# Kernel tuning notes

Measured on AMD Instinct MI355X. Metric: run time of the kernel, lower is better.

## Reference

```python
import jax, jax.numpy as jnp
import numpy as np

# ---- static config (mirrors HashEncoderHyFluid.__init__) ----
MIN_RES = np.array([16, 16, 16, 16], dtype=np.float64)
MAX_RES = np.array([256, 256, 256, 128], dtype=np.float64)
NUM_SCALES = 16
MAX_PARAMS = 2 ** 19
F = 2  # features_per_level
N_QUERIES = 1_000_000
PRIMES = np.array([1, 2654435761, 805459861, 3674653429], dtype=np.uint32)
# 16 corner offsets of the 4D hypercube, bit d of idx selects low/high along dim d
BITS = np.array([[(i >> d) & 1 for d in range(4)] for i in range(16)], dtype=np.int32)  # (16,4)


def build_config():
    b = np.exp((np.log(MAX_RES) - np.log(MIN_RES)) / (NUM_SCALES - 1))
    shapes, sizes, indicators, offsets = [], [], [], []
    total = 0
    for s in range(NUM_SCALES):
        res = np.ceil(MIN_RES * np.power(b, s)).astype(np.int64)
        raw = int(res[0] + 1) * int(res[1] + 1) * int(res[2] + 1) * int(res[3] + 1)
        p = raw if raw % 8 == 0 else ((raw + 7) // 8) * 8
        p = min(MAX_PARAMS, p)
        shapes.append(res)
        sizes.append(p)
        indicators.append(1 if raw <= p else 0)
        offsets.append(total)
        total += p * F
    return shapes, sizes, indicators, offsets, total


SHAPES, SIZES, INDICATORS, OFFSETS, TOTAL_HASH_SIZE = build_config()  # total = 15205344


def setup_inputs() -> dict:
    key = jax.random.key(0)
    k1, k2 = jax.random.split(key)
    xyzt = jax.random.uniform(k1, (N_QUERIES, 4), dtype=jnp.float32)  # coords in [0,1)
    hash_table = (jax.random.uniform(k2, (TOTAL_HASH_SIZE,), dtype=jnp.float32) * 2.0 - 1.0) * 0.001
    return {"xyzt": xyzt, "hash_table": hash_table}


def _encode_scale(xyzt, hash_table, res, size, indicator, offset):
    # xyzt: (N,4) in [0,1]; res: np int64 (4,)
    resf = jnp.asarray(res.astype(np.float32))
    pos = xyzt * resf                      # (N,4) grid-space position
    grid = jnp.floor(pos)
    frac = pos - grid                      # (N,4)
    grid = grid.astype(jnp.int32)
    corners = grid[:, None, :] + jnp.asarray(BITS)[None, :, :]          # (N,16,4)
    hi = jnp.asarray(BITS, jnp.float32)[None, :, :]                     # (1,16,4)
    w = jnp.prod(hi * frac[:, None, :] + (1.0 - hi) * (1.0 - frac[:, None, :]), axis=-1)  # (N,16)
    cu = corners.astype(jnp.uint32)
    if indicator == 1:
        # dense linear indexing: strides = cumprod(res+1), wrapping at uint32 like taichi
        strides = np.cumprod(np.concatenate([[1], (res + 1)[:3]])).astype(np.uint32)
        idx = jnp.sum(cu * jnp.asarray(strides), axis=-1)               # (N,16) uint32, wraps
    else:
        # xor hash with large primes
        h = cu[..., 0] * jnp.uint32(PRIMES[0])
        for d in range(1, 4):
            h = h ^ (cu[..., d] * jnp.uint32(PRIMES[d]))
        idx = h
    idx = (idx % jnp.uint32(size)).astype(jnp.int32)
    base = offset + idx * F                                             # (N,16)
    feats = hash_table[base[..., None] + jnp.arange(F)]                 # (N,16,F)
    return jnp.einsum("nc,ncf->nf", w, feats)                           # (N,F)


def reference(xyzt, hash_table):
    outs = []
    for s in range(NUM_SCALES):
        outs.append(_encode_scale(xyzt, hash_table, SHAPES[s], SIZES[s], INDICATORS[s], OFFSETS[s]))
    return jnp.concatenate(outs, axis=-1)  # (N, NUM_SCALES * F)
```

## Files before the change

kernel.cpp:

```cpp
#include <hip/hip_runtime.h>
#include <cstdint>
#include <cmath>


#define NSCALES 16
#define TPB 256
#define BINS 65536

struct Cfg {
  float    res[NSCALES][4];
  uint32_t key[NSCALES][4];
  uint32_t mask[NSCALES];
  int      offset[NSCALES];
  int      dense[NSCALES];
};

typedef float v4f __attribute__((ext_vector_type(4)));
typedef float v2f __attribute__((ext_vector_type(2)));

__device__ __forceinline__ uint32_t bucket_key(float x, float y, float z, float w)
{
  uint32_t bx = (uint32_t)(x * 16.f); bx = bx > 15u ? 15u : bx;
  uint32_t by = (uint32_t)(y * 16.f); by = by > 15u ? 15u : by;
  uint32_t bz = (uint32_t)(z * 16.f); bz = bz > 15u ? 15u : bz;
  uint32_t bt = (uint32_t)(w * 16.f); bt = bt > 15u ? 15u : bt;
  uint32_t k = 0;
#pragma unroll
  for (int b = 0; b < 4; ++b) {
    k |= ((bx >> b) & 1u) << (4 * b + 0);
    k |= ((by >> b) & 1u) << (4 * b + 1);
    k |= ((bz >> b) & 1u) << (4 * b + 2);
    k |= ((bt >> b) & 1u) << (4 * b + 3);
  }
  return k;
}

__global__ __launch_bounds__(TPB) void hist_kernel(
    const float* __restrict__ xyzt, uint32_t* __restrict__ hist, int N)
{
  const int i = blockIdx.x * TPB + threadIdx.x;
  if (i >= N) return;
  const v4f c = *(reinterpret_cast<const v4f*>(xyzt) + i);
  atomicAdd(&hist[bucket_key(c.x, c.y, c.z, c.w)], 1u);
}

__global__ __launch_bounds__(256) void scan_kernel(
    const uint32_t* __restrict__ hist, uint32_t* __restrict__ boff)
{
  __shared__ uint32_t part[256];
  const int t = threadIdx.x;
  const int base = t * (BINS / 256);
  uint32_t s = 0;
  for (int j = 0; j < BINS / 256; ++j) s += hist[base + j];
  part[t] = s;
  __syncthreads();
  for (int off = 1; off < 256; off <<= 1) {
    uint32_t v = (t >= off) ? part[t - off] : 0u;
    __syncthreads();
    part[t] += v;
    __syncthreads();
  }
  uint32_t run = part[t] - s;
  for (int j = 0; j < BINS / 256; ++j) {
    boff[base + j] = run;
    run += hist[base + j];
  }
}

__global__ __launch_bounds__(TPB) void scatter_kernel(
    const float* __restrict__ xyzt,
    const uint32_t* __restrict__ boff, uint32_t* __restrict__ cur,
    uint32_t* __restrict__ perm, float* __restrict__ c_sorted, int N)
{
  const int i = blockIdx.x * TPB + threadIdx.x;
  if (i >= N) return;
  const v4f c = *(reinterpret_cast<const v4f*>(xyzt) + i);
  const uint32_t k = bucket_key(c.x, c.y, c.z, c.w);
  const uint32_t pos = boff[k] + atomicAdd(&cur[k], 1u);
  perm[pos] = (uint32_t)i;
  *(reinterpret_cast<v4f*>(c_sorted) + pos) = c;
}

__global__ __launch_bounds__(TPB) void gather_kernel(
    const float*  __restrict__ coords,
    const float*  __restrict__ table,
    float2*       __restrict__ ws,
    int N, Cfg cfg)
{
  const int s = blockIdx.y;
  const int q = blockIdx.x * TPB + threadIdx.x;
  if (q >= N) return;
  const v4f c = *(reinterpret_cast<const v4f*>(coords) + q);

  const float rx = cfg.res[s][0], ry = cfg.res[s][1];
  const float rz = cfg.res[s][2], rw = cfg.res[s][3];
  const uint32_t K0 = cfg.key[s][0], K1 = cfg.key[s][1];
  const uint32_t K2 = cfg.key[s][2], K3 = cfg.key[s][3];

  const float px = c.x * rx, py = c.y * ry, pz = c.z * rz, pw = c.w * rw;
  const float gx = floorf(px), gy = floorf(py), gz = floorf(pz), gw = floorf(pw);
  const float fx = px - gx, fy = py - gy, fz = pz - gz, fw = pw - gw;
  const uint32_t ix = (uint32_t)(int)gx, iy = (uint32_t)(int)gy;
  const uint32_t iz = (uint32_t)(int)gz, iw = (uint32_t)(int)gw;

  const uint32_t x0 = ix * K0, x1 = x0 + K0;
  const uint32_t y0 = iy * K1, y1 = y0 + K1;
  const uint32_t z0 = iz * K2, z1 = z0 + K2;
  const uint32_t u0 = iw * K3, u1 = u0 + K3;

  const float wx0 = 1.f - fx, wy0 = 1.f - fy, wz0 = 1.f - fz, ww0 = 1.f - fw;
  const float wA[4] = { wx0 * wy0, fx * wy0, wx0 * fy, fx * fy };
  const float wB[4] = { wz0 * ww0, fz * ww0, wz0 * fw, fz * fw };

  const float*  tbf = table + cfg.offset[s];
  const float2* __restrict__ tb  = reinterpret_cast<const float2*>(tbf);
  const float4* __restrict__ tb4 = reinterpret_cast<const float4*>(tbf);

  float a0 = 0.f, a1 = 0.f;
  if (cfg.dense[s]) {
    const uint32_t hA[4] = { x0 + y0, x1 + y0, x0 + y1, x1 + y1 };
    const uint32_t hB[4] = { z0 + u0, z1 + u0, z0 + u1, z1 + u1 };
#pragma unroll
    for (int i = 0; i < 16; ++i) {
      const uint32_t idx = hA[i & 3] + hB[i >> 2];
      const float2 v = tb[idx];
      const float w = wA[i & 3] * wB[i >> 2];
      a0 = fmaf(w, v.x, a0);
      a1 = fmaf(w, v.y, a1);
    }
  } else {
    const uint32_t msk = cfg.mask[s];
    if ((ix & 1u) == 0u) {
      const uint32_t yv[2] = { y0, y1 };
      const uint32_t zw[4] = { z0 ^ u0, z1 ^ u0, z0 ^ u1, z1 ^ u1 };
#pragma unroll
      for (int j = 0; j < 8; ++j) {
        const int jy = j & 1, jz = j >> 1;
        const uint32_t p  = (x0 ^ yv[jy] ^ zw[jz]) & msk;
        const uint32_t e  = p & ~1u;
        const uint32_t sel = p & 1u;
        const float4 v = tb4[e >> 1];
        const float wlo = wA[2 * jy]     * wB[jz];
        const float whi = wA[2 * jy + 1] * wB[jz];
        const float l0 = sel ? v.z : v.x, l1 = sel ? v.w : v.y;
        const float h0 = sel ? v.x : v.z, h1 = sel ? v.y : v.w;
        a0 = fmaf(wlo, l0, fmaf(whi, h0, a0));
        a1 = fmaf(wlo, l1, fmaf(whi, h1, a1));
      }
    } else {
      const uint32_t hA[4] = { x0 ^ y0, x1 ^ y0, x0 ^ y1, x1 ^ y1 };
      const uint32_t hB[4] = { z0 ^ u0, z1 ^ u0, z0 ^ u1, z1 ^ u1 };
#pragma unroll
      for (int i = 0; i < 16; ++i) {
        const uint32_t idx = (hA[i & 3] ^ hB[i >> 2]) & msk;
        const float2 v = tb[idx];
        const float w = wA[i & 3] * wB[i >> 2];
        a0 = fmaf(w, v.x, a0);
        a1 = fmaf(w, v.y, a1);
      }
    }
  }
  v2f val = { a0, a1 };
  __builtin_nontemporal_store(val, (v2f*)&ws[(size_t)s * N + q]);
}

__global__ __launch_bounds__(TPB) void transpose_direct(
    const float2*   __restrict__ ws,
    const uint32_t* __restrict__ perm,
    float*          __restrict__ out,
    int N)
{
  const int g = blockIdx.x * TPB + threadIdx.x;
  if (g >= N * 8) return;
  const int q  = g >> 3;
  const int l8 = g & 7;
  const int s0 = l8 * 2;
  const float2 a = ws[(size_t)s0 * N + q];
  const float2 b = ws[(size_t)(s0 + 1) * N + q];
  const uint32_t pq = perm[q];
  v4f val = { a.x, a.y, b.x, b.y };
  __builtin_nontemporal_store(val, (v4f*)(out + (size_t)pq * 32 + l8 * 4));
}

__global__ __launch_bounds__(TPB) void transpose_kernel(
    const float2* __restrict__ ws,
    float*        __restrict__ out,
    int N)
{
  __shared__ float2 st[NSCALES][TPB + 1];
  const int t  = threadIdx.x;
  const int q  = blockIdx.x * TPB + t;
  const int ql = q < N ? q : N - 1;
#pragma unroll
  for (int s = 0; s < NSCALES; ++s)
    st[s][t] = ws[(size_t)s * N + ql];
  __syncthreads();
  const int base = blockIdx.x * (TPB * 2 * NSCALES);
#pragma unroll
  for (int it = 0; it < 8; ++it) {
    const int G  = it * 1024 + t * 4;
    const int qi = G >> 5;
    const int s0 = (G & 31) >> 1;
    if (blockIdx.x * TPB + qi < N) {
      const float2 a = st[s0][qi];
      const float2 b = st[s0 + 1][qi];
      v4f val = { a.x, a.y, b.x, b.y };
      __builtin_nontemporal_store(val, (v4f*)(out + base + G));
    }
  }
}

__global__ __launch_bounds__(TPB) void hashenc_fused(
    const float4* __restrict__ xyzt,
    const float*  __restrict__ table,
    float*        __restrict__ out,
    int N, Cfg cfg)
{
  __shared__ float2 st[NSCALES][TPB + 1];
  const int t  = threadIdx.x;
  const int q  = blockIdx.x * TPB + t;
  const int ql = q < N ? q : N - 1;
  const float4 c = xyzt[ql];
#pragma unroll 1
  for (int s = 0; s < NSCALES; ++s) {
    const float rx = cfg.res[s][0], ry = cfg.res[s][1];
    const float rz = cfg.res[s][2], rw = cfg.res[s][3];
    const uint32_t K0 = cfg.key[s][0], K1 = cfg.key[s][1];
    const uint32_t K2 = cfg.key[s][2], K3 = cfg.key[s][3];
    const float px = c.x * rx, py = c.y * ry, pz = c.z * rz, pw = c.w * rw;
    const float gx = floorf(px), gy = floorf(py), gz = floorf(pz), gw = floorf(pw);
    const float fx = px - gx, fy = py - gy, fz = pz - gz, fw = pw - gw;
    const uint32_t ix = (uint32_t)(int)gx, iy = (uint32_t)(int)gy;
    const uint32_t iz = (uint32_t)(int)gz, iw = (uint32_t)(int)gw;
    const uint32_t x0 = ix * K0, x1 = x0 + K0;
    const uint32_t y0 = iy * K1, y1 = y0 + K1;
    const uint32_t z0 = iz * K2, z1 = z0 + K2;
    const uint32_t u0 = iw * K3, u1 = u0 + K3;
    const float wx0 = 1.f - fx, wy0 = 1.f - fy, wz0 = 1.f - fz, ww0 = 1.f - fw;
    const float wA[4] = { wx0 * wy0, fx * wy0, wx0 * fy, fx * fy };
    const float wB[4] = { wz0 * ww0, fz * ww0, wz0 * fw, fz * fw };
    const float2* __restrict__ tb =
        reinterpret_cast<const float2*>(table + cfg.offset[s]);
    float a0 = 0.f, a1 = 0.f;
    if (cfg.dense[s]) {
      const uint32_t hA[4] = { x0 + y0, x1 + y0, x0 + y1, x1 + y1 };
      const uint32_t hB[4] = { z0 + u0, z1 + u0, z0 + u1, z1 + u1 };
#pragma unroll
      for (int i = 0; i < 16; ++i) {
        const uint32_t idx = hA[i & 3] + hB[i >> 2];
        const float2 v = tb[idx];
        const float w = wA[i & 3] * wB[i >> 2];
        a0 = fmaf(w, v.x, a0); a1 = fmaf(w, v.y, a1);
      }
    } else {
      const uint32_t msk = cfg.mask[s];
      const uint32_t hA[4] = { x0 ^ y0, x1 ^ y0, x0 ^ y1, x1 ^ y1 };
      const uint32_t hB[4] = { z0 ^ u0, z1 ^ u0, z0 ^ u1, z1 ^ u1 };
#pragma unroll
      for (int i = 0; i < 16; ++i) {
        const uint32_t idx = (hA[i & 3] ^ hB[i >> 2]) & msk;
        const float2 v = tb[idx];
        const float w = wA[i & 3] * wB[i >> 2];
        a0 = fmaf(w, v.x, a0); a1 = fmaf(w, v.y, a1);
      }
    }
    st[s][t] = make_float2(a0, a1);
  }
  __syncthreads();
  const int base = blockIdx.x * (TPB * 2 * NSCALES);
#pragma unroll
  for (int it = 0; it < 8; ++it) {
    const int G  = it * 1024 + t * 4;
    const int qi = G >> 5;
    const int s0 = (G & 31) >> 1;
    if (blockIdx.x * TPB + qi < N) {
      const float2 a = st[s0][qi];
      const float2 b = st[s0 + 1][qi];
      v4f val = { a.x, a.y, b.x, b.y };
      __builtin_nontemporal_store(val, (v4f*)(out + base + G));
    }
  }
}

static void build_cfg(Cfg& cfg)
{
  const double minr[4] = { 16.0, 16.0, 16.0, 16.0 };
  const double maxr[4] = { 256.0, 256.0, 256.0, 128.0 };
  const uint32_t primes[4] = { 1u, 2654435761u, 805459861u, 3674653429u };

  double b[4];
  for (int d = 0; d < 4; ++d)
    b[d] = ::exp((::log(maxr[d]) - ::log(minr[d])) / (double)(NSCALES - 1));

  long long total = 0;
  for (int s = 0; s < NSCALES; ++s) {
    long long res[4];
    for (int d = 0; d < 4; ++d)
      res[d] = (long long)::ceil(minr[d] * ::pow(b[d], (double)s));

    const long long raw =
        (res[0] + 1) * (res[1] + 1) * (res[2] + 1) * (res[3] + 1);
    long long p = (raw % 8 == 0) ? raw : ((raw + 7) / 8) * 8;
    if (p > 524288) p = 524288;
    const int ind = (raw <= p) ? 1 : 0;

    for (int d = 0; d < 4; ++d) cfg.res[s][d] = (float)res[d];
    if (ind) {
      cfg.key[s][0] = 1u;
      cfg.key[s][1] = (uint32_t)(res[0] + 1);
      cfg.key[s][2] = (uint32_t)((res[0] + 1) * (res[1] + 1));
      cfg.key[s][3] = (uint32_t)((res[0] + 1) * (res[1] + 1) * (res[2] + 1));
    } else {
      for (int d = 0; d < 4; ++d) cfg.key[s][d] = primes[d];
    }
    cfg.mask[s]   = (uint32_t)(p - 1);
    cfg.offset[s] = (int)total;
    cfg.dense[s]  = ind;
    total += p * 2;
  }
}

static inline size_t align_up(size_t v, size_t a) { return (v + a - 1) & ~(a - 1); }

extern "C" void kernel_launch(void* const* d_in, const int* in_sizes, int n_in,
                              void* d_out, int out_size, void* d_ws, size_t ws_size,
                              hipStream_t stream)
{
  const float* xyzt  = (const float*)d_in[0];
  const float* table = (const float*)d_in[1];
  float*       out   = (float*)d_out;
  const int N = in_sizes[0] / 4;

  Cfg cfg;
  build_cfg(cfg);

  const int qblocks = (N + TPB - 1) / TPB;

  size_t off = 0;
  const size_t perm_off = off;             off = align_up(off + (size_t)N * 4, 256);
  const size_t hist_off = off;             off = align_up(off + (size_t)BINS * 4, 256);
  const size_t cur_off  = off;             off = align_up(off + (size_t)BINS * 4, 256);
  const size_t boff_off = off;             off = align_up(off + (size_t)BINS * 4, 256);
  const size_t cs_off   = align_up(off, 16);  off = cs_off + (size_t)N * 16;
  const size_t ws_off   = align_up(off, 16);
  const size_t need_sorted = ws_off + (size_t)N * NSCALES * sizeof(float2);
  const size_t need_plain  = (size_t)N * NSCALES * sizeof(float2);

  char* wsb = (char*)d_ws;

  if (ws_size >= need_sorted) {
    uint32_t* perm = (uint32_t*)(wsb + perm_off);
    uint32_t* hist = (uint32_t*)(wsb + hist_off);
    uint32_t* cur  = (uint32_t*)(wsb + cur_off);
    uint32_t* boff = (uint32_t*)(wsb + boff_off);
    float*    csrt = (float*)(wsb + cs_off);
    float2*   ws   = (float2*)(wsb + ws_off);

    hipMemsetAsync(hist, 0, (size_t)BINS * 4, stream);
    hipMemsetAsync(cur,  0, (size_t)BINS * 4, stream);
    hipLaunchKernelGGL(hist_kernel, dim3(qblocks), dim3(TPB), 0, stream,
                       xyzt, hist, N);
    hipLaunchKernelGGL(scan_kernel, dim3(1), dim3(256), 0, stream, hist, boff);
    hipLaunchKernelGGL(scatter_kernel, dim3(qblocks), dim3(TPB), 0, stream,
                       xyzt, boff, cur, perm, csrt, N);
    hipLaunchKernelGGL(gather_kernel, dim3(qblocks, NSCALES), dim3(TPB), 0,
                       stream, csrt, table, ws, N, cfg);
    const int tblocks = (N * 8 + TPB - 1) / TPB;
    hipLaunchKernelGGL(transpose_direct, dim3(tblocks), dim3(TPB), 0, stream,
                       ws, perm, out, N);
  } else if (ws_size >= need_plain) {
    float2* ws = (float2*)d_ws;
    hipLaunchKernelGGL(gather_kernel, dim3(qblocks, NSCALES), dim3(TPB), 0,
                       stream, xyzt, table, ws, N, cfg);
    hipLaunchKernelGGL(transpose_kernel, dim3(qblocks), dim3(TPB), 0,
                       stream, ws, out, N);
  } else {
    hipLaunchKernelGGL(hashenc_fused, dim3(qblocks), dim3(TPB), 0,
                       stream, (const float4*)xyzt, table, out, N, cfg);
  }
}
```

Before: 841.0 us.

## Batch gather loads, stage transpose through LDS, widen scan, merge memsets

The gather kernel now computes all corner indices and issues all table loads before any accumulation, which exposes more memory-level parallelism at the cost of more live registers. The permuted transpose stages 128 queries across all scales in shared memory, so the reads from the workspace are coalesced before the scattered 16-byte output stores. The scan uses 1024 threads, the hist and cur buffers are placed next to each other so one memset clears both, and the gather output store becomes a plain store instead of a nontemporal one. An s_base parameter is added but always passed as 0.

```diff
diff --git a/kernel.cpp b/kernel.cpp
--- a/kernel.cpp
+++ b/kernel.cpp
@@ -6,6 +6,7 @@
 #define NSCALES 16
 #define TPB 256
 #define BINS 65536
+#define QPB 128
 
 struct Cfg {
   float    res[NSCALES][4];
@@ -44,24 +45,24 @@
   atomicAdd(&hist[bucket_key(c.x, c.y, c.z, c.w)], 1u);
 }
 
-__global__ __launch_bounds__(256) void scan_kernel(
+__global__ __launch_bounds__(1024) void scan_kernel(
     const uint32_t* __restrict__ hist, uint32_t* __restrict__ boff)
 {
-  __shared__ uint32_t part[256];
+  __shared__ uint32_t part[1024];
   const int t = threadIdx.x;
-  const int base = t * (BINS / 256);
+  const int base = t * (BINS / 1024);
   uint32_t s = 0;
-  for (int j = 0; j < BINS / 256; ++j) s += hist[base + j];
+  for (int j = 0; j < BINS / 1024; ++j) s += hist[base + j];
   part[t] = s;
   __syncthreads();
-  for (int off = 1; off < 256; off <<= 1) {
+  for (int off = 1; off < 1024; off <<= 1) {
     uint32_t v = (t >= off) ? part[t - off] : 0u;
     __syncthreads();
     part[t] += v;
     __syncthreads();
   }
   uint32_t run = part[t] - s;
-  for (int j = 0; j < BINS / 256; ++j) {
+  for (int j = 0; j < BINS / 1024; ++j) {
     boff[base + j] = run;
     run += hist[base + j];
   }
@@ -85,9 +86,9 @@
     const float*  __restrict__ coords,
     const float*  __restrict__ table,
     float2*       __restrict__ ws,
-    int N, Cfg cfg)
-{
-  const int s = blockIdx.y;
+    int N, int s_base, Cfg cfg)
+{
+  const int s = (int)blockIdx.y + s_base;
   const int q = blockIdx.x * TPB + threadIdx.x;
   if (q >= N) return;
   const v4f c = *(reinterpret_cast<const v4f*>(coords) + q);
@@ -120,66 +121,93 @@
   if (cfg.dense[s]) {
     const uint32_t hA[4] = { x0 + y0, x1 + y0, x0 + y1, x1 + y1 };
     const uint32_t hB[4] = { z0 + u0, z1 + u0, z0 + u1, z1 + u1 };
+    uint32_t idx[16];
+#pragma unroll
+    for (int i = 0; i < 16; ++i) idx[i] = hA[i & 3] + hB[i >> 2];
+    float2 v[16];
+#pragma unroll
+    for (int i = 0; i < 16; ++i) v[i] = tb[idx[i]];
 #pragma unroll
     for (int i = 0; i < 16; ++i) {
-      const uint32_t idx = hA[i & 3] + hB[i >> 2];
-      const float2 v = tb[idx];
       const float w = wA[i & 3] * wB[i >> 2];
-      a0 = fmaf(w, v.x, a0);
-      a1 = fmaf(w, v.y, a1);
+      a0 = fmaf(w, v[i].x, a0);
+      a1 = fmaf(w, v[i].y, a1);
     }
   } else {
     const uint32_t msk = cfg.mask[s];
     if ((ix & 1u) == 0u) {
       const uint32_t yv[2] = { y0, y1 };
       const uint32_t zw[4] = { z0 ^ u0, z1 ^ u0, z0 ^ u1, z1 ^ u1 };
+      uint32_t p[8];
+#pragma unroll
+      for (int j = 0; j < 8; ++j)
+        p[j] = (x0 ^ yv[j & 1] ^ zw[j >> 1]) & msk;
+      float4 v[8];
+#pragma unroll
+      for (int j = 0; j < 8; ++j) v[j] = tb4[p[j] >> 1];
 #pragma unroll
       for (int j = 0; j < 8; ++j) {
         const int jy = j & 1, jz = j >> 1;
-        const uint32_t p  = (x0 ^ yv[jy] ^ zw[jz]) & msk;
-        const uint32_t e  = p & ~1u;
-        const uint32_t sel = p & 1u;
-        const float4 v = tb4[e >> 1];
+        const uint32_t sel = p[j] & 1u;
         const float wlo = wA[2 * jy]     * wB[jz];
         const float whi = wA[2 * jy + 1] * wB[jz];
-        const float l0 = sel ? v.z : v.x, l1 = sel ? v.w : v.y;
-        const float h0 = sel ? v.x : v.z, h1 = sel ? v.y : v.w;
+        const float l0 = sel ? v[j].z : v[j].x, l1 = sel ? v[j].w : v[j].y;
+        const float h0 = sel ? v[j].x : v[j].z, h1 = sel ? v[j].y : v[j].w;
         a0 = fmaf(wlo, l0, fmaf(whi, h0, a0));
         a1 = fmaf(wlo, l1, fmaf(whi, h1, a1));
       }
     } else {
       const uint32_t hA[4] = { x0 ^ y0, x1 ^ y0, x0 ^ y1, x1 ^ y1 };
       const uint32_t hB[4] = { z0 ^ u0, z1 ^ u0, z0 ^ u1, z1 ^ u1 };
+      uint32_t idx[16];
+#pragma unroll
+      for (int i = 0; i < 16; ++i) idx[i] = (hA[i & 3] ^ hB[i >> 2]) & msk;
+      float2 v[16];
+#pragma unroll
+      for (int i = 0; i < 16; ++i) v[i] = tb[idx[i]];
 #pragma unroll
       for (int i = 0; i < 16; ++i) {
-        const uint32_t idx = (hA[i & 3] ^ hB[i >> 2]) & msk;
-        const float2 v = tb[idx];
         const float w = wA[i & 3] * wB[i >> 2];
-        a0 = fmaf(w, v.x, a0);
-        a1 = fmaf(w, v.y, a1);
+        a0 = fmaf(w, v[i].x, a0);
+        a1 = fmaf(w, v[i].y, a1);
       }
     }
   }
-  v2f val = { a0, a1 };
-  __builtin_nontemporal_store(val, (v2f*)&ws[(size_t)s * N + q]);
-}
-
-__global__ __launch_bounds__(TPB) void transpose_direct(
+  ws[(size_t)s * N + q] = make_float2(a0, a1);
+}
+
+__global__ __launch_bounds__(TPB) void transpose_perm(
     const float2*   __restrict__ ws,
     const uint32_t* __restrict__ perm,
     float*          __restrict__ out,
     int N)
 {
-  const int g = blockIdx.x * TPB + threadIdx.x;
-  if (g >= N * 8) return;
-  const int q  = g >> 3;
-  const int l8 = g & 7;
-  const int s0 = l8 * 2;
-  const float2 a = ws[(size_t)s0 * N + q];
-  const float2 b = ws[(size_t)(s0 + 1) * N + q];
-  const uint32_t pq = perm[q];
-  v4f val = { a.x, a.y, b.x, b.y };
-  __builtin_nontemporal_store(val, (v4f*)(out + (size_t)pq * 32 + l8 * 4));
+  __shared__ float2 st[NSCALES][QPB + 1];
+  const int t  = threadIdx.x;
+  const int q0 = blockIdx.x * QPB;
+#pragma unroll
+  for (int i = 0; i < (NSCALES * QPB) / TPB; ++i) {
+    const int idx = i * TPB + t;
+    const int sc  = idx >> 7;
+    const int qi  = idx & (QPB - 1);
+    const int q   = q0 + qi;
+    st[sc][qi] = ws[(size_t)sc * N + (q < N ? q : N - 1)];
+  }
+  __syncthreads();
+#pragma unroll
+  for (int i = 0; i < (QPB * 8) / TPB; ++i) {
+    const int g  = i * TPB + t;
+    const int qi = g >> 3;
+    const int h  = g & 7;
+    const int q  = q0 + qi;
+    if (q < N) {
+      const float2 a = st[2 * h][qi];
+      const float2 b = st[2 * h + 1][qi];
+      const uint32_t pq = perm[q];
+      v4f val = { a.x, a.y, b.x, b.y };
+      __builtin_nontemporal_store(val, (v4f*)(out + (size_t)pq * 32 + h * 4));
+    }
+  }
 }
 
 __global__ __launch_bounds__(TPB) void transpose_kernel(
@@ -338,7 +366,7 @@
 
   size_t off = 0;
   const size_t perm_off = off;             off = align_up(off + (size_t)N * 4, 256);
-  const size_t hist_off = off;             off = align_up(off + (size_t)BINS * 4, 256);
+  const size_t hist_off = off;             off += (size_t)BINS * 4;
   const size_t cur_off  = off;             off = align_up(off + (size_t)BINS * 4, 256);
   const size_t boff_off = off;             off = align_up(off + (size_t)BINS * 4, 256);
   const size_t cs_off   = align_up(off, 16);  off = cs_off + (size_t)N * 16;
@@ -356,22 +384,21 @@
     float*    csrt = (float*)(wsb + cs_off);
     float2*   ws   = (float2*)(wsb + ws_off);
 
-    hipMemsetAsync(hist, 0, (size_t)BINS * 4, stream);
-    hipMemsetAsync(cur,  0, (size_t)BINS * 4, stream);
+    hipMemsetAsync(hist, 0, (size_t)BINS * 8, stream);
     hipLaunchKernelGGL(hist_kernel, dim3(qblocks), dim3(TPB), 0, stream,
                        xyzt, hist, N);
-    hipLaunchKernelGGL(scan_kernel, dim3(1), dim3(256), 0, stream, hist, boff);
+    hipLaunchKernelGGL(scan_kernel, dim3(1), dim3(1024), 0, stream, hist, boff);
     hipLaunchKernelGGL(scatter_kernel, dim3(qblocks), dim3(TPB), 0, stream,
                        xyzt, boff, cur, perm, csrt, N);
     hipLaunchKernelGGL(gather_kernel, dim3(qblocks, NSCALES), dim3(TPB), 0,
-                       stream, csrt, table, ws, N, cfg);
-    const int tblocks = (N * 8 + TPB - 1) / TPB;
-    hipLaunchKernelGGL(transpose_direct, dim3(tblocks), dim3(TPB), 0, stream,
+                       stream, csrt, table, ws, N, 0, cfg);
+    const int tblocks = (N + QPB - 1) / QPB;
+    hipLaunchKernelGGL(transpose_perm, dim3(tblocks), dim3(TPB), 0, stream,
                        ws, perm, out, N);
   } else if (ws_size >= need_plain) {
     float2* ws = (float2*)d_ws;
     hipLaunchKernelGGL(gather_kernel, dim3(qblocks, NSCALES), dim3(TPB), 0,
-                       stream, xyzt, table, ws, N, cfg);
+                       stream, xyzt, table, ws, N, 0, cfg);
     hipLaunchKernelGGL(transpose_kernel, dim3(qblocks), dim3(TPB), 0,
                        stream, ws, out, N);
   } else {
```

Measured after the change: 811.2 us. -3.5%, faster.
